# Kernel optimization log

Hardware: AMD Instinct MI355X
Metric: run time of the kernel (lower is better)

Reference implementation:

```python
import jax, jax.numpy as jnp
import numpy as np

DIM_M = 512
NEG_INF = -1e30


def setup_inputs() -> dict:
    key = jax.random.key(0)
    k1, k2, k3, k4, k5, k6, k7 = jax.random.split(key, 7)
    B, Lc, Lq, d = 16, 1024, 512, DIM_M
    C = jax.random.normal(k1, (B, Lc, d), dtype=jnp.float32)
    Q = jax.random.normal(k2, (B, Lq, d), dtype=jnp.float32)
    cmask = jax.random.randint(k3, (B, Lc), 0, 2).astype(jnp.float32)
    qmask = jax.random.randint(k4, (B, Lq), 0, 2).astype(jnp.float32)
    lim = np.sqrt(1.0 / d)
    w = jax.random.uniform(k5, (3 * d,), minval=-lim, maxval=lim, dtype=jnp.float32)
    # out_linear: Linear(4d -> d), torch default init
    bound = np.sqrt(1.0 / (4 * d))
    out_w = jax.random.uniform(k6, (d, 4 * d), minval=-bound, maxval=bound, dtype=jnp.float32)
    out_b = jax.random.uniform(k7, (d,), minval=-bound, maxval=bound, dtype=jnp.float32)
    return {"C": C, "Q": Q, "cmask": cmask, "qmask": qmask, "w": w, "out_w": out_w, "out_b": out_b}


def _mask_logits(t, m):
    return t * m + (1.0 - m) * NEG_INF


def reference(C, Q, cmask, qmask, w, out_w, out_b):
    d = C.shape[-1]
    w1, w2, w3 = w[:d], w[d:2 * d], w[2 * d:]
    # Decomposed trilinear similarity (same math as cat([Ct,Qt,Ct*Qt]) @ w):
    # S[b,i,j] = C[b,i]@w1 + Q[b,j]@w2 + (C[b,i]*w3) @ Q[b,j]
    S = (C @ w1)[:, :, None] + (Q @ w2)[:, None, :] \
        + jnp.einsum('bid,bjd->bij', C * w3, Q)  # [B, Lc, Lq]
    qm = qmask[:, None, :]  # [B, 1, Lq]
    cm = cmask[:, :, None]  # [B, Lc, 1]
    S1 = jax.nn.softmax(_mask_logits(S, qm), axis=2)  # over Lq
    S2 = jax.nn.softmax(_mask_logits(S, cm), axis=1)  # over Lc
    A = jnp.einsum('bij,bjd->bid', S1, Q)  # [B, Lc, d]
    # bmm(bmm(S1, S2^T), C) == S1 @ (S2^T @ C) by associativity (cheaper)
    S2TC = jnp.einsum('bij,bid->bjd', S2, C)  # [B, Lq, d]
    Bm = jnp.einsum('bij,bjd->bid', S1, S2TC)  # [B, Lc, d]
    out = jnp.concatenate([C, A, C * A, C * Bm], axis=2)  # [B, Lc, 4d]
    # dropout inactive (inference); out_linear
    return out @ out_w.T + out_b
```

## Files before the change

### kernel.cpp

```cpp
#include <hip/hip_runtime.h>
#include <hip/hip_bf16.h>


#define NB 16
#define LC 1024
#define LQ 512
#define DM 512
#define D4 2048
#define NEGINF (-1e30f)
#define BK 32
#define LDAp 40

typedef __bf16 v8bf __attribute__((ext_vector_type(8)));
typedef __bf16 v4bf __attribute__((ext_vector_type(4)));
typedef float  v4f  __attribute__((ext_vector_type(4)));

#define MFMA16 __builtin_amdgcn_mfma_f32_16x16x32_bf16

#define TILE_SETUP8 \
  const int t = threadIdx.x, lane = t & 63, wave = t >> 6; \
  const int wm = wave >> 2, wn = wave & 3, quad = lane >> 4, col = lane & 15; \
  const int sr = t >> 2, skc = (t & 3) * 8;

#define ZERO_ACC8 \
  v4f acc[4][2]; \
  _Pragma("unroll") for (int x = 0; x < 4; ++x) \
  _Pragma("unroll") for (int y = 0; y < 2; ++y) \
  _Pragma("unroll") for (int r = 0; r < 4; ++r) acc[x][y][r] = 0.f;

#define FRAG_MMA8(AL, BL) do { \
  v8bf af_[4], bf_[2]; \
  _Pragma("unroll") for (int x = 0; x < 4; ++x) \
    af_[x] = *(const v8bf*)&AL[(wm * 64 + x * 16 + col) * LDAp + quad * 8]; \
  _Pragma("unroll") for (int y = 0; y < 2; ++y) \
    bf_[y] = *(const v8bf*)&BL[(wn * 32 + y * 16 + col) * LDAp + quad * 8]; \
  _Pragma("unroll") for (int x = 0; x < 4; ++x) \
  _Pragma("unroll") for (int y = 0; y < 2; ++y) \
    acc[x][y] = MFMA16(af_[x], bf_[y], acc[x][y], 0, 0, 0); \
} while (0)

__device__ __forceinline__ void xcd_remap(int& bx, int& by, int& bz) {
  const int gx = gridDim.x, gy = gridDim.y, gz = gridDim.z;
  int flat = bx + gx * (by + gy * bz);
  int per = (gx * gy * gz) >> 3;
  int nw = (flat & 7) * per + (flat >> 3);
  bx = nw % gx;
  int r = nw / gx;
  by = r % gy;
  bz = r / gy;
}

__device__ __forceinline__ v8bf cvt8(const float* p) {
  float4 f0 = *(const float4*)p, f1 = *(const float4*)(p + 4);
  v8bf h;
  h[0] = (__bf16)f0.x; h[1] = (__bf16)f0.y; h[2] = (__bf16)f0.z; h[3] = (__bf16)f0.w;
  h[4] = (__bf16)f1.x; h[5] = (__bf16)f1.y; h[6] = (__bf16)f1.z; h[7] = (__bf16)f1.w;
  return h;
}

__global__ void k_rowdots(const float* __restrict__ C, const float* __restrict__ Q,
                          const float* __restrict__ w,
                          float* __restrict__ cw1, float* __restrict__ qw2) {
  const int wid = threadIdx.x >> 6, lane = threadIdx.x & 63;
  const int row = blockIdx.x * 4 + wid;
  const bool isC = row < NB * LC;
  const float* src = isC ? (C + (size_t)row * DM) : (Q + (size_t)(row - NB * LC) * DM);
  const float* wv  = isC ? w : (w + DM);
  float v = 0.f;
#pragma unroll
  for (int tt = 0; tt < 8; ++tt) {
    int k = lane + 64 * tt;
    v += src[k] * wv[k];
  }
#pragma unroll
  for (int off = 32; off; off >>= 1) v += __shfl_down(v, off, 64);
  if (lane == 0) {
    if (isC) cw1[row] = v;
    else     qw2[row - NB * LC] = v;
  }
}

__global__ void k_transpose(const float* __restrict__ in, __bf16* __restrict__ outT,
                            int R, int Cd) {
  __shared__ __bf16 tile[64][66];
  const int b = blockIdx.z;
  const int r0 = blockIdx.y * 64, c0 = blockIdx.x * 64;
  const int tr = threadIdx.x >> 6, tc = threadIdx.x & 63;
  const float* inb = in + (size_t)b * R * Cd;
  __bf16* outb = outT + (size_t)b * Cd * R;
  for (int r = tr; r < 64; r += 4)
    tile[r][tc] = (__bf16)inb[(size_t)(r0 + r) * Cd + c0 + tc];
  __syncthreads();
  for (int c = tr; c < 64; c += 4)
    outb[(size_t)(c0 + c) * R + r0 + tc] = tile[tc][c];
}

__global__ __launch_bounds__(512) void k_mfma_S(
    const float* __restrict__ C, const float* __restrict__ Q, const float* __restrict__ w,
    const float* __restrict__ cw1, const float* __restrict__ qw2, float* __restrict__ S) {
  __shared__ __bf16 Al[128 * LDAp], Bl[128 * LDAp];
  int bx = blockIdx.x, by = blockIdx.y, bz = blockIdx.z;
  xcd_remap(bx, by, bz);
  const int b = bz, i0 = by * 128, j0 = bx * 128;
  TILE_SETUP8
  const float* Cb = C + (size_t)b * LC * DM;
  const float* Qb = Q + (size_t)b * LQ * DM;
  const float* w3 = w + 2 * DM;
  ZERO_ACC8
  for (int k0 = 0; k0 < DM; k0 += BK) {
    const float* ca = Cb + (size_t)(i0 + sr) * DM + k0 + skc;
    const float* qa = Qb + (size_t)(j0 + sr) * DM + k0 + skc;
    const float* wa = w3 + k0 + skc;
    float4 c0 = *(const float4*)ca, c1 = *(const float4*)(ca + 4);
    float4 w0 = *(const float4*)wa, w1 = *(const float4*)(wa + 4);
    v8bf ah;
    ah[0] = (__bf16)(c0.x * w0.x); ah[1] = (__bf16)(c0.y * w0.y);
    ah[2] = (__bf16)(c0.z * w0.z); ah[3] = (__bf16)(c0.w * w0.w);
    ah[4] = (__bf16)(c1.x * w1.x); ah[5] = (__bf16)(c1.y * w1.y);
    ah[6] = (__bf16)(c1.z * w1.z); ah[7] = (__bf16)(c1.w * w1.w);
    *(v8bf*)&Al[sr * LDAp + skc] = ah;
    *(v8bf*)&Bl[sr * LDAp + skc] = cvt8(qa);
    __syncthreads();
    FRAG_MMA8(Al, Bl);
    __syncthreads();
  }
  float* Sb = S + (size_t)b * LC * LQ;
#pragma unroll
  for (int x = 0; x < 4; ++x) {
    const int mB = i0 + wm * 64 + x * 16 + quad * 4;
    float cv[4];
#pragma unroll
    for (int r = 0; r < 4; ++r) cv[r] = cw1[b * LC + mB + r];
#pragma unroll
    for (int y = 0; y < 2; ++y) {
      const int j = j0 + wn * 32 + y * 16 + col;
      const float qv = qw2[b * LQ + j];
#pragma unroll
      for (int r = 0; r < 4; ++r)
        Sb[(size_t)(mB + r) * LQ + j] = acc[x][y][r] + cv[r] + qv;
    }
  }
}

__global__ __launch_bounds__(1024) void k_softstat(
    const float* __restrict__ S, const float* __restrict__ qmask,
    const float* __restrict__ cmask, __bf16* __restrict__ S1,
    float2* __restrict__ pstat) {
  __shared__ float2 cst[16][LQ];
  const int b = blockIdx.y, ic = blockIdx.x;
  const int tid = threadIdx.x, wv = tid >> 6, lane = tid & 63;
  const float* qm  = qmask + b * LQ;
  const float* cm  = cmask + b * LC + ic * 64;
  const float* Sb  = S  + ((size_t)b * LC + ic * 64) * LQ;
  __bf16*      S1b = S1 + ((size_t)b * LC + ic * 64) * LQ;
  float colm[8], cols[8];
#pragma unroll
  for (int tt = 0; tt < 8; ++tt) { colm[tt] = -3e38f; cols[tt] = 0.f; }
  for (int it = 0; it < 4; ++it) {
    const int r = wv * 4 + it;
    const float cmv = cm[r];
    const float* Srow = Sb + (size_t)r * LQ;
    float sv[8], l1[8];
    float m = -3e38f;
#pragma unroll
    for (int tt = 0; tt < 8; ++tt) {
      int j = lane + 64 * tt;
      sv[tt] = Srow[j];
      float qv = qm[j];
      l1[tt] = qv * sv[tt] + (1.f - qv) * NEGINF;
      m = fmaxf(m, l1[tt]);
    }
#pragma unroll
    for (int off = 32; off; off >>= 1) m = fmaxf(m, __shfl_xor(m, off, 64));
    float e[8], s = 0.f;
#pragma unroll
    for (int tt = 0; tt < 8; ++tt) { e[tt] = __expf(l1[tt] - m); s += e[tt]; }
#pragma unroll
    for (int off = 32; off; off >>= 1) s += __shfl_xor(s, off, 64);
    const float inv = 1.f / s;
#pragma unroll
    for (int tt = 0; tt < 8; ++tt)
      S1b[(size_t)r * LQ + lane + 64 * tt] = (__bf16)(e[tt] * inv);
#pragma unroll
    for (int tt = 0; tt < 8; ++tt) {
      float l2 = cmv * sv[tt] + (1.f - cmv) * NEGINF;
      if (l2 > colm[tt]) { cols[tt] *= __expf(colm[tt] - l2); colm[tt] = l2; }
      cols[tt] += __expf(l2 - colm[tt]);
    }
  }
#pragma unroll
  for (int tt = 0; tt < 8; ++tt) cst[wv][lane + 64 * tt] = make_float2(colm[tt], cols[tt]);
  __syncthreads();
  if (tid < LQ) {
    float M = -3e38f, Sd = 0.f;
#pragma unroll
    for (int k = 0; k < 16; ++k) {
      float2 p = cst[k][tid];
      float nM = fmaxf(M, p.x);
      Sd = Sd * __expf(M - nM) + p.y * __expf(p.x - nM);
      M = nM;
    }
    pstat[((size_t)(b * 16 + ic) * LQ) + tid] = make_float2(M, Sd);
  }
}

__global__ void k_colwrite(const float* __restrict__ S, const float* __restrict__ cmask,
                           const float2* __restrict__ pstat, __bf16* __restrict__ S2T) {
  __shared__ float Mf[64], If[64];
  __shared__ __bf16 tile[64][66];
  const int b = blockIdx.z, ic = blockIdx.y, j0 = blockIdx.x * 64;
  const int c = threadIdx.x & 63, ip = threadIdx.x >> 6;
  if (threadIdx.x < 64) {
    float M = -3e38f, Sd = 0.f;
#pragma unroll
    for (int k = 0; k < 16; ++k) {
      float2 p = pstat[((size_t)(b * 16 + k) * LQ) + j0 + threadIdx.x];
      float nM = fmaxf(M, p.x);
      Sd = Sd * __expf(M - nM) + p.y * __expf(p.x - nM);
      M = nM;
    }
    Mf[threadIdx.x] = M; If[threadIdx.x] = 1.f / Sd;
  }
  __syncthreads();
  const float M = Mf[c], inv = If[c];
  const float* Sb = S + ((size_t)b * LC + ic * 64) * LQ;
  const float* cm = cmask + b * LC + ic * 64;
  for (int r = ip; r < 64; r += 4) {
    float mk = cm[r];
    float logit = mk * Sb[(size_t)r * LQ + j0 + c] + (1.f - mk) * NEGINF;
    tile[r][c] = (__bf16)(__expf(logit - M) * inv);
  }
  __syncthreads();
  __bf16* S2Tb = S2T + ((size_t)b * LQ + j0) * LC + ic * 64;
  for (int jr = ip; jr < 64; jr += 4)
    S2Tb[(size_t)jr * LC + c] = tile[c][jr];
}

__global__ __launch_bounds__(512) void k_mfma_A(
    const __bf16* __restrict__ S1, const __bf16* __restrict__ QT, __bf16* __restrict__ Aw) {
  __shared__ __bf16 Al[128 * LDAp], Bl[128 * LDAp];
  int bx = blockIdx.x, by = blockIdx.y, bz = blockIdx.z;
  xcd_remap(bx, by, bz);
  const int b = bz, i0 = by * 128, n0 = bx * 128;
  TILE_SETUP8
  const __bf16* S1b = S1 + (size_t)b * LC * LQ;
  const __bf16* QTb = QT + (size_t)b * DM * LQ;
  ZERO_ACC8
  for (int k0 = 0; k0 < LQ; k0 += BK) {
    *(v8bf*)&Al[sr * LDAp + skc] = *(const v8bf*)(S1b + (size_t)(i0 + sr) * LQ + k0 + skc);
    *(v8bf*)&Bl[sr * LDAp + skc] = *(const v8bf*)(QTb + (size_t)(n0 + sr) * LQ + k0 + skc);
    __syncthreads();
    FRAG_MMA8(Al, Bl);
    __syncthreads();
  }
  __bf16* Ab = Aw + (size_t)b * LC * DM;
#pragma unroll
  for (int x = 0; x < 4; ++x) {
    const int mB = i0 + wm * 64 + x * 16 + quad * 4;
#pragma unroll
    for (int y = 0; y < 2; ++y) {
      const int n = n0 + wn * 32 + y * 16 + col;
#pragma unroll
      for (int r = 0; r < 4; ++r)
        Ab[(size_t)(mB + r) * DM + n] = (__bf16)acc[x][y][r];
    }
  }
}

__global__ __launch_bounds__(512) void k_mfma_T(
    const __bf16* __restrict__ S2T, const __bf16* __restrict__ CT, __bf16* __restrict__ S2TCT) {
  __shared__ __bf16 Al[128 * LDAp], Bl[128 * LDAp];
  int bx = blockIdx.x, by = blockIdx.y, bz = blockIdx.z;
  xcd_remap(bx, by, bz);
  const int b = bz, j0 = by * 128, n0 = bx * 128;
  TILE_SETUP8
  const __bf16* S2Tb = S2T + (size_t)b * LQ * LC;
  const __bf16* CTb  = CT  + (size_t)b * DM * LC;
  ZERO_ACC8
  for (int k0 = 0; k0 < LC; k0 += BK) {
    *(v8bf*)&Al[sr * LDAp + skc] = *(const v8bf*)(S2Tb + (size_t)(j0 + sr) * LC + k0 + skc);
    *(v8bf*)&Bl[sr * LDAp + skc] = *(const v8bf*)(CTb  + (size_t)(n0 + sr) * LC + k0 + skc);
    __syncthreads();
    FRAG_MMA8(Al, Bl);
    __syncthreads();
  }
#pragma unroll
  for (int x = 0; x < 4; ++x) {
    const int jB = j0 + wm * 64 + x * 16 + quad * 4;
#pragma unroll
    for (int y = 0; y < 2; ++y) {
      const int n = n0 + wn * 32 + y * 16 + col;
      v4bf h;
#pragma unroll
      for (int r = 0; r < 4; ++r) h[r] = (__bf16)acc[x][y][r];
      *(v4bf*)&S2TCT[((size_t)b * DM + n) * LQ + jB] = h;
    }
  }
}

__global__ __launch_bounds__(512) void k_mfma_Bm(
    const __bf16* __restrict__ S1, const __bf16* __restrict__ S2TCT, __bf16* __restrict__ Bmw) {
  __shared__ __bf16 Al[128 * LDAp], Bl[128 * LDAp];
  int bx = blockIdx.x, by = blockIdx.y, bz = blockIdx.z;
  xcd_remap(bx, by, bz);
  const int b = bz, i0 = by * 128, n0 = bx * 128;
  TILE_SETUP8
  const __bf16* S1b = S1 + (size_t)b * LC * LQ;
  const __bf16* Tb  = S2TCT + (size_t)b * DM * LQ;
  ZERO_ACC8
  for (int k0 = 0; k0 < LQ; k0 += BK) {
    *(v8bf*)&Al[sr * LDAp + skc] = *(const v8bf*)(S1b + (size_t)(i0 + sr) * LQ + k0 + skc);
    *(v8bf*)&Bl[sr * LDAp + skc] = *(const v8bf*)(Tb  + (size_t)(n0 + sr) * LQ + k0 + skc);
    __syncthreads();
    FRAG_MMA8(Al, Bl);
    __syncthreads();
  }
  __bf16* Bb = Bmw + (size_t)b * LC * DM;
#pragma unroll
  for (int x = 0; x < 4; ++x) {
    const int mB = i0 + wm * 64 + x * 16 + quad * 4;
#pragma unroll
    for (int y = 0; y < 2; ++y) {
      const int n = n0 + wn * 32 + y * 16 + col;
#pragma unroll
      for (int r = 0; r < 4; ++r)
        Bb[(size_t)(mB + r) * DM + n] = (__bf16)acc[x][y][r];
    }
  }
}

__global__ __launch_bounds__(512) void k_mfma_out(
    const float* __restrict__ C, const __bf16* __restrict__ Aw, const __bf16* __restrict__ Bmw,
    const float* __restrict__ OW, const float* __restrict__ ob, float* __restrict__ out) {
  __shared__ __bf16 Asg[2][128 * LDAp], Bsg[2][128 * LDAp];
  int bx = blockIdx.x, by = blockIdx.y, bz = blockIdx.z;
  xcd_remap(bx, by, bz);
  const int b = bz, i0 = by * 128, n0 = bx * 128;
  TILE_SETUP8
  const float*  Cb = C   + (size_t)b * LC * DM;
  const __bf16* Ab = Aw  + (size_t)b * LC * DM;
  const __bf16* Bb = Bmw + (size_t)b * LC * DM;
  ZERO_ACC8
#pragma unroll
  for (int pass = 0; pass < 2; ++pass) {
    for (int kl0 = 0; kl0 < DM; kl0 += BK) {
      const float*  cr = Cb + (size_t)(i0 + sr) * DM + kl0 + skc;
      const __bf16* ap = Ab + (size_t)(i0 + sr) * DM + kl0 + skc;
      const int off = sr * LDAp + skc;
      v8bf av = *(const v8bf*)ap;
      if (pass == 0) {
        *(v8bf*)&Asg[0][off] = cvt8(cr);
        *(v8bf*)&Asg[1][off] = av;
      } else {
        float4 f0 = *(const float4*)cr, f1 = *(const float4*)(cr + 4);
        v8bf bv = *(const v8bf*)(Bb + (size_t)(i0 + sr) * DM + kl0 + skc);
        float cf[8] = {f0.x, f0.y, f0.z, f0.w, f1.x, f1.y, f1.z, f1.w};
        v8bf hCA, hCB;
#pragma unroll
        for (int e = 0; e < 8; ++e) {
          hCA[e] = (__bf16)(cf[e] * (float)av[e]);
          hCB[e] = (__bf16)(cf[e] * (float)bv[e]);
        }
        *(v8bf*)&Asg[0][off] = hCA;
        *(v8bf*)&Asg[1][off] = hCB;
      }
      const float* owr = OW + (size_t)(n0 + sr) * D4 + pass * 2 * DM + kl0 + skc;
      *(v8bf*)&Bsg[0][off] = cvt8(owr);
      *(v8bf*)&Bsg[1][off] = cvt8(owr + DM);
      __syncthreads();
      FRAG_MMA8(Asg[0], Bsg[0]);
      FRAG_MMA8(Asg[1], Bsg[1]);
      __syncthreads();
    }
  }
  float* outb = out + (size_t)b * LC * DM;
#pragma unroll
  for (int x = 0; x < 4; ++x) {
    const int mB = i0 + wm * 64 + x * 16 + quad * 4;
#pragma unroll
    for (int y = 0; y < 2; ++y) {
      const int n = n0 + wn * 32 + y * 16 + col;
      const float bv = ob[n];
#pragma unroll
      for (int r = 0; r < 4; ++r)
        outb[(size_t)(mB + r) * DM + n] = acc[x][y][r] + bv;
    }
  }
}

extern "C" void kernel_launch(void* const* d_in, const int* in_sizes, int n_in,
                              void* d_out, int out_size, void* d_ws, size_t ws_size,
                              hipStream_t stream) {
  const float* C     = (const float*)d_in[0];
  const float* Q     = (const float*)d_in[1];
  const float* cmask = (const float*)d_in[2];
  const float* qmask = (const float*)d_in[3];
  const float* w     = (const float*)d_in[4];
  const float* out_w = (const float*)d_in[5];
  const float* out_b = (const float*)d_in[6];
  float* out = (float*)d_out;

  char* base = (char*)d_ws;
  float*  cw1   = (float*)base;
  float*  qw2   = (float*)(base + 65536);
  char*   R     = base + 131072;
  float*  S     = (float*)R;
  __bf16* Aw    = (__bf16*)R;
  __bf16* CT    = (__bf16*)(R + (16u << 20));
  __bf16* Bmw   = (__bf16*)(R + (16u << 20));
  __bf16* S1    = (__bf16*)(base + 131072 + (32u << 20));
  __bf16* S2T   = (__bf16*)(base + 131072 + (48u << 20));
  char*   Z     = base + 131072 + (64u << 20);
  float2* pstat = (float2*)Z;
  __bf16* QT    = (__bf16*)Z;
  __bf16* S2TCT = (__bf16*)Z;
  (void)in_sizes; (void)n_in; (void)out_size; (void)ws_size;

  k_rowdots<<<(NB * LC + NB * LQ) / 4, 256, 0, stream>>>(C, Q, w, cw1, qw2);
  k_mfma_S<<<dim3(LQ / 128, LC / 128, NB), 512, 0, stream>>>(C, Q, w, cw1, qw2, S);
  k_softstat<<<dim3(LC / 64, NB), 1024, 0, stream>>>(S, qmask, cmask, S1, pstat);
  k_colwrite<<<dim3(LQ / 64, LC / 64, NB), 256, 0, stream>>>(S, cmask, pstat, S2T);
  k_transpose<<<dim3(DM / 64, LQ / 64, NB), 256, 0, stream>>>(Q, QT, LQ, DM);
  k_transpose<<<dim3(DM / 64, LC / 64, NB), 256, 0, stream>>>(C, CT, LC, DM);
  k_mfma_A<<<dim3(DM / 128, LC / 128, NB), 512, 0, stream>>>(S1, QT, Aw);
  k_mfma_T<<<dim3(DM / 128, LQ / 128, NB), 512, 0, stream>>>(S2T, CT, S2TCT);
  k_mfma_Bm<<<dim3(DM / 128, LC / 128, NB), 512, 0, stream>>>(S1, S2TCT, Bmw);
  k_mfma_out<<<dim3(DM / 128, LC / 128, NB), 512, 0, stream>>>(C, Aw, Bmw, out_w, out_b, out);
}
```

Measured before the change: 299.1 us.

## Prefetch next K-tile into registers, widen K-step, pre-convert out_w to bf16

The MFMA GEMM kernels now load the next K-slice from global memory into registers while the current slice is being computed, which overlaps load latency with MFMA work. The S, A, T and Bm kernels move to a 64-wide K step with a larger LDS stride, so they need half as many barriers. The output GEMM is restructured into a single loop over four LDS buffers and reads out_w from a bf16 copy that a new kernel writes into the S2T workspace once S2T is no longer needed. In exchange, the kernels use more registers and more LDS, and each call pays for an extra conversion launch.

```diff
diff --git a/kernel.cpp b/kernel.cpp
--- a/kernel.cpp
+++ b/kernel.cpp
@@ -8,8 +8,8 @@
 #define DM 512
 #define D4 2048
 #define NEGINF (-1e30f)
-#define BK 32
-#define LDAp 40
+#define LDA64 72
+#define LDA32 40
 
 typedef __bf16 v8bf __attribute__((ext_vector_type(8)));
 typedef __bf16 v4bf __attribute__((ext_vector_type(4)));
@@ -20,7 +20,7 @@
 #define TILE_SETUP8 \
   const int t = threadIdx.x, lane = t & 63, wave = t >> 6; \
   const int wm = wave >> 2, wn = wave & 3, quad = lane >> 4, col = lane & 15; \
-  const int sr = t >> 2, skc = (t & 3) * 8;
+  const int sr = t >> 2;
 
 #define ZERO_ACC8 \
   v4f acc[4][2]; \
@@ -28,12 +28,12 @@
   _Pragma("unroll") for (int y = 0; y < 2; ++y) \
   _Pragma("unroll") for (int r = 0; r < 4; ++r) acc[x][y][r] = 0.f;
 
-#define FRAG_MMA8(AL, BL) do { \
+#define FRAG_MMA8S(AL, BL, LDA, KO) do { \
   v8bf af_[4], bf_[2]; \
   _Pragma("unroll") for (int x = 0; x < 4; ++x) \
-    af_[x] = *(const v8bf*)&AL[(wm * 64 + x * 16 + col) * LDAp + quad * 8]; \
+    af_[x] = *(const v8bf*)&AL[(wm * 64 + x * 16 + col) * LDA + KO + quad * 8]; \
   _Pragma("unroll") for (int y = 0; y < 2; ++y) \
-    bf_[y] = *(const v8bf*)&BL[(wn * 32 + y * 16 + col) * LDAp + quad * 8]; \
+    bf_[y] = *(const v8bf*)&BL[(wn * 32 + y * 16 + col) * LDA + KO + quad * 8]; \
   _Pragma("unroll") for (int x = 0; x < 4; ++x) \
   _Pragma("unroll") for (int y = 0; y < 2; ++y) \
     acc[x][y] = MFMA16(af_[x], bf_[y], acc[x][y], 0, 0, 0); \
@@ -50,11 +50,10 @@
   bz = r / gy;
 }
 
-__device__ __forceinline__ v8bf cvt8(const float* p) {
-  float4 f0 = *(const float4*)p, f1 = *(const float4*)(p + 4);
+__device__ __forceinline__ v8bf cvt8f(float4 a, float4 b) {
   v8bf h;
-  h[0] = (__bf16)f0.x; h[1] = (__bf16)f0.y; h[2] = (__bf16)f0.z; h[3] = (__bf16)f0.w;
-  h[4] = (__bf16)f1.x; h[5] = (__bf16)f1.y; h[6] = (__bf16)f1.z; h[7] = (__bf16)f1.w;
+  h[0] = (__bf16)a.x; h[1] = (__bf16)a.y; h[2] = (__bf16)a.z; h[3] = (__bf16)a.w;
+  h[4] = (__bf16)b.x; h[5] = (__bf16)b.y; h[6] = (__bf16)b.z; h[7] = (__bf16)b.w;
   return h;
 }
 
@@ -95,33 +94,56 @@
     outb[(size_t)(c0 + c) * R + r0 + tc] = tile[tc][c];
 }
 
+__global__ void k_owcvt(const float* __restrict__ OW, __bf16* __restrict__ OWb) {
+  size_t i = ((size_t)blockIdx.x * 256 + threadIdx.x) * 4;
+  float4 f = *(const float4*)(OW + i);
+  v4bf h; h[0] = (__bf16)f.x; h[1] = (__bf16)f.y; h[2] = (__bf16)f.z; h[3] = (__bf16)f.w;
+  *(v4bf*)(OWb + i) = h;
+}
+
 __global__ __launch_bounds__(512) void k_mfma_S(
     const float* __restrict__ C, const float* __restrict__ Q, const float* __restrict__ w,
     const float* __restrict__ cw1, const float* __restrict__ qw2, float* __restrict__ S) {
-  __shared__ __bf16 Al[128 * LDAp], Bl[128 * LDAp];
+  __shared__ __bf16 Al[128 * LDA64], Bl[128 * LDA64];
   int bx = blockIdx.x, by = blockIdx.y, bz = blockIdx.z;
   xcd_remap(bx, by, bz);
   const int b = bz, i0 = by * 128, j0 = bx * 128;
   TILE_SETUP8
+  const int skc = (t & 3) * 16;
   const float* Cb = C + (size_t)b * LC * DM;
   const float* Qb = Q + (size_t)b * LQ * DM;
   const float* w3 = w + 2 * DM;
-  ZERO_ACC8
-  for (int k0 = 0; k0 < DM; k0 += BK) {
+  float4 pc[4], pq[4];
+  auto load = [&](int k0) {
     const float* ca = Cb + (size_t)(i0 + sr) * DM + k0 + skc;
     const float* qa = Qb + (size_t)(j0 + sr) * DM + k0 + skc;
+#pragma unroll
+    for (int u = 0; u < 4; ++u) {
+      pc[u] = *(const float4*)(ca + 4 * u);
+      pq[u] = *(const float4*)(qa + 4 * u);
+    }
+  };
+  load(0);
+  ZERO_ACC8
+  for (int k0 = 0; k0 < DM; k0 += 64) {
     const float* wa = w3 + k0 + skc;
-    float4 c0 = *(const float4*)ca, c1 = *(const float4*)(ca + 4);
-    float4 w0 = *(const float4*)wa, w1 = *(const float4*)(wa + 4);
-    v8bf ah;
-    ah[0] = (__bf16)(c0.x * w0.x); ah[1] = (__bf16)(c0.y * w0.y);
-    ah[2] = (__bf16)(c0.z * w0.z); ah[3] = (__bf16)(c0.w * w0.w);
-    ah[4] = (__bf16)(c1.x * w1.x); ah[5] = (__bf16)(c1.y * w1.y);
-    ah[6] = (__bf16)(c1.z * w1.z); ah[7] = (__bf16)(c1.w * w1.w);
-    *(v8bf*)&Al[sr * LDAp + skc] = ah;
-    *(v8bf*)&Bl[sr * LDAp + skc] = cvt8(qa);
-    __syncthreads();
-    FRAG_MMA8(Al, Bl);
+#pragma unroll
+    for (int u = 0; u < 2; ++u) {
+      float4 c0 = pc[2 * u], c1 = pc[2 * u + 1];
+      float4 w0 = *(const float4*)(wa + 8 * u), w1 = *(const float4*)(wa + 8 * u + 4);
+      v8bf ah;
+      ah[0] = (__bf16)(c0.x * w0.x); ah[1] = (__bf16)(c0.y * w0.y);
+      ah[2] = (__bf16)(c0.z * w0.z); ah[3] = (__bf16)(c0.w * w0.w);
+      ah[4] = (__bf16)(c1.x * w1.x); ah[5] = (__bf16)(c1.y * w1.y);
+      ah[6] = (__bf16)(c1.z * w1.z); ah[7] = (__bf16)(c1.w * w1.w);
+      *(v8bf*)&Al[sr * LDA64 + skc + 8 * u] = ah;
+      *(v8bf*)&Bl[sr * LDA64 + skc + 8 * u] = cvt8f(pq[2 * u], pq[2 * u + 1]);
+    }
+    __syncthreads();
+    int kn = k0 + 64; if (kn >= DM) kn = 0;
+    load(kn);
+    FRAG_MMA8S(Al, Bl, LDA64, 0);
+    FRAG_MMA8S(Al, Bl, LDA64, 32);
     __syncthreads();
   }
   float* Sb = S + (size_t)b * LC * LQ;
@@ -238,19 +260,29 @@
 
 __global__ __launch_bounds__(512) void k_mfma_A(
     const __bf16* __restrict__ S1, const __bf16* __restrict__ QT, __bf16* __restrict__ Aw) {
-  __shared__ __bf16 Al[128 * LDAp], Bl[128 * LDAp];
+  __shared__ __bf16 Al[128 * LDA64], Bl[128 * LDA64];
   int bx = blockIdx.x, by = blockIdx.y, bz = blockIdx.z;
   xcd_remap(bx, by, bz);
   const int b = bz, i0 = by * 128, n0 = bx * 128;
   TILE_SETUP8
-  const __bf16* S1b = S1 + (size_t)b * LC * LQ;
-  const __bf16* QTb = QT + (size_t)b * DM * LQ;
+  const int skc = (t & 3) * 16;
+  const __bf16* Ar = S1 + (size_t)b * LC * LQ + (size_t)(i0 + sr) * LQ + skc;
+  const __bf16* Br = QT + (size_t)b * DM * LQ + (size_t)(n0 + sr) * LQ + skc;
+  v8bf pa0, pa1, pb0, pb1;
+  auto load = [&](int k0) {
+    pa0 = *(const v8bf*)(Ar + k0); pa1 = *(const v8bf*)(Ar + k0 + 8);
+    pb0 = *(const v8bf*)(Br + k0); pb1 = *(const v8bf*)(Br + k0 + 8);
+  };
+  load(0);
   ZERO_ACC8
-  for (int k0 = 0; k0 < LQ; k0 += BK) {
-    *(v8bf*)&Al[sr * LDAp + skc] = *(const v8bf*)(S1b + (size_t)(i0 + sr) * LQ + k0 + skc);
-    *(v8bf*)&Bl[sr * LDAp + skc] = *(const v8bf*)(QTb + (size_t)(n0 + sr) * LQ + k0 + skc);
-    __syncthreads();
-    FRAG_MMA8(Al, Bl);
+  for (int k0 = 0; k0 < LQ; k0 += 64) {
+    *(v8bf*)&Al[sr * LDA64 + skc] = pa0; *(v8bf*)&Al[sr * LDA64 + skc + 8] = pa1;
+    *(v8bf*)&Bl[sr * LDA64 + skc] = pb0; *(v8bf*)&Bl[sr * LDA64 + skc + 8] = pb1;
+    __syncthreads();
+    int kn = k0 + 64; if (kn >= LQ) kn = 0;
+    load(kn);
+    FRAG_MMA8S(Al, Bl, LDA64, 0);
+    FRAG_MMA8S(Al, Bl, LDA64, 32);
     __syncthreads();
   }
   __bf16* Ab = Aw + (size_t)b * LC * DM;
@@ -269,19 +301,29 @@
 
 __global__ __launch_bounds__(512) void k_mfma_T(
     const __bf16* __restrict__ S2T, const __bf16* __restrict__ CT, __bf16* __restrict__ S2TCT) {
-  __shared__ __bf16 Al[128 * LDAp], Bl[128 * LDAp];
+  __shared__ __bf16 Al[128 * LDA64], Bl[128 * LDA64];
   int bx = blockIdx.x, by = blockIdx.y, bz = blockIdx.z;
   xcd_remap(bx, by, bz);
   const int b = bz, j0 = by * 128, n0 = bx * 128;
   TILE_SETUP8
-  const __bf16* S2Tb = S2T + (size_t)b * LQ * LC;
-  const __bf16* CTb  = CT  + (size_t)b * DM * LC;
+  const int skc = (t & 3) * 16;
+  const __bf16* Ar = S2T + (size_t)b * LQ * LC + (size_t)(j0 + sr) * LC + skc;
+  const __bf16* Br = CT  + (size_t)b * DM * LC + (size_t)(n0 + sr) * LC + skc;
+  v8bf pa0, pa1, pb0, pb1;
+  auto load = [&](int k0) {
+    pa0 = *(const v8bf*)(Ar + k0); pa1 = *(const v8bf*)(Ar + k0 + 8);
+    pb0 = *(const v8bf*)(Br + k0); pb1 = *(const v8bf*)(Br + k0 + 8);
+  };
+  load(0);
   ZERO_ACC8
-  for (int k0 = 0; k0 < LC; k0 += BK) {
-    *(v8bf*)&Al[sr * LDAp + skc] = *(const v8bf*)(S2Tb + (size_t)(j0 + sr) * LC + k0 + skc);
-    *(v8bf*)&Bl[sr * LDAp + skc] = *(const v8bf*)(CTb  + (size_t)(n0 + sr) * LC + k0 + skc);
-    __syncthreads();
-    FRAG_MMA8(Al, Bl);
+  for (int k0 = 0; k0 < LC; k0 += 64) {
+    *(v8bf*)&Al[sr * LDA64 + skc] = pa0; *(v8bf*)&Al[sr * LDA64 + skc + 8] = pa1;
+    *(v8bf*)&Bl[sr * LDA64 + skc] = pb0; *(v8bf*)&Bl[sr * LDA64 + skc + 8] = pb1;
+    __syncthreads();
+    int kn = k0 + 64; if (kn >= LC) kn = 0;
+    load(kn);
+    FRAG_MMA8S(Al, Bl, LDA64, 0);
+    FRAG_MMA8S(Al, Bl, LDA64, 32);
     __syncthreads();
   }
 #pragma unroll
@@ -300,19 +342,29 @@
 
 __global__ __launch_bounds__(512) void k_mfma_Bm(
     const __bf16* __restrict__ S1, const __bf16* __restrict__ S2TCT, __bf16* __restrict__ Bmw) {
-  __shared__ __bf16 Al[128 * LDAp], Bl[128 * LDAp];
+  __shared__ __bf16 Al[128 * LDA64], Bl[128 * LDA64];
   int bx = blockIdx.x, by = blockIdx.y, bz = blockIdx.z;
   xcd_remap(bx, by, bz);
   const int b = bz, i0 = by * 128, n0 = bx * 128;
   TILE_SETUP8
-  const __bf16* S1b = S1 + (size_t)b * LC * LQ;
-  const __bf16* Tb  = S2TCT + (size_t)b * DM * LQ;
+  const int skc = (t & 3) * 16;
+  const __bf16* Ar = S1    + (size_t)b * LC * LQ + (size_t)(i0 + sr) * LQ + skc;
+  const __bf16* Br = S2TCT + (size_t)b * DM * LQ + (size_t)(n0 + sr) * LQ + skc;
+  v8bf pa0, pa1, pb0, pb1;
+  auto load = [&](int k0) {
+    pa0 = *(const v8bf*)(Ar + k0); pa1 = *(const v8bf*)(Ar + k0 + 8);
+    pb0 = *(const v8bf*)(Br + k0); pb1 = *(const v8bf*)(Br + k0 + 8);
+  };
+  load(0);
   ZERO_ACC8
-  for (int k0 = 0; k0 < LQ; k0 += BK) {
-    *(v8bf*)&Al[sr * LDAp + skc] = *(const v8bf*)(S1b + (size_t)(i0 + sr) * LQ + k0 + skc);
-    *(v8bf*)&Bl[sr * LDAp + skc] = *(const v8bf*)(Tb  + (size_t)(n0 + sr) * LQ + k0 + skc);
-    __syncthreads();
-    FRAG_MMA8(Al, Bl);
+  for (int k0 = 0; k0 < LQ; k0 += 64) {
+    *(v8bf*)&Al[sr * LDA64 + skc] = pa0; *(v8bf*)&Al[sr * LDA64 + skc + 8] = pa1;
+    *(v8bf*)&Bl[sr * LDA64 + skc] = pb0; *(v8bf*)&Bl[sr * LDA64 + skc + 8] = pb1;
+    __syncthreads();
+    int kn = k0 + 64; if (kn >= LQ) kn = 0;
+    load(kn);
+    FRAG_MMA8S(Al, Bl, LDA64, 0);
+    FRAG_MMA8S(Al, Bl, LDA64, 32);
     __syncthreads();
   }
   __bf16* Bb = Bmw + (size_t)b * LC * DM;
@@ -331,47 +383,49 @@
 
 __global__ __launch_bounds__(512) void k_mfma_out(
     const float* __restrict__ C, const __bf16* __restrict__ Aw, const __bf16* __restrict__ Bmw,
-    const float* __restrict__ OW, const float* __restrict__ ob, float* __restrict__ out) {
-  __shared__ __bf16 Asg[2][128 * LDAp], Bsg[2][128 * LDAp];
+    const __bf16* __restrict__ OWb, const float* __restrict__ ob, float* __restrict__ out) {
+  __shared__ __bf16 Asg[4][128 * LDA32], Bsg[4][128 * LDA32];
   int bx = blockIdx.x, by = blockIdx.y, bz = blockIdx.z;
   xcd_remap(bx, by, bz);
   const int b = bz, i0 = by * 128, n0 = bx * 128;
   TILE_SETUP8
-  const float*  Cb = C   + (size_t)b * LC * DM;
-  const __bf16* Ab = Aw  + (size_t)b * LC * DM;
-  const __bf16* Bb = Bmw + (size_t)b * LC * DM;
+  const int skc = (t & 3) * 8;
+  const float*  Cr = C   + (size_t)b * LC * DM + (size_t)(i0 + sr) * DM + skc;
+  const __bf16* Ar = Aw  + (size_t)b * LC * DM + (size_t)(i0 + sr) * DM + skc;
+  const __bf16* Br = Bmw + (size_t)b * LC * DM + (size_t)(i0 + sr) * DM + skc;
+  const __bf16* Wr = OWb + (size_t)(n0 + sr) * D4 + skc;
+  float4 pc0, pc1; v8bf pA, pB, pw[4];
+  auto load = [&](int kl) {
+    pc0 = *(const float4*)(Cr + kl); pc1 = *(const float4*)(Cr + kl + 4);
+    pA = *(const v8bf*)(Ar + kl);
+    pB = *(const v8bf*)(Br + kl);
+#pragma unroll
+    for (int s = 0; s < 4; ++s) pw[s] = *(const v8bf*)(Wr + s * DM + kl);
+  };
+  load(0);
   ZERO_ACC8
-#pragma unroll
-  for (int pass = 0; pass < 2; ++pass) {
-    for (int kl0 = 0; kl0 < DM; kl0 += BK) {
-      const float*  cr = Cb + (size_t)(i0 + sr) * DM + kl0 + skc;
-      const __bf16* ap = Ab + (size_t)(i0 + sr) * DM + kl0 + skc;
-      const int off = sr * LDAp + skc;
-      v8bf av = *(const v8bf*)ap;
-      if (pass == 0) {
-        *(v8bf*)&Asg[0][off] = cvt8(cr);
-        *(v8bf*)&Asg[1][off] = av;
-      } else {
-        float4 f0 = *(const float4*)cr, f1 = *(const float4*)(cr + 4);
-        v8bf bv = *(const v8bf*)(Bb + (size_t)(i0 + sr) * DM + kl0 + skc);
-        float cf[8] = {f0.x, f0.y, f0.z, f0.w, f1.x, f1.y, f1.z, f1.w};
-        v8bf hCA, hCB;
-#pragma unroll
-        for (int e = 0; e < 8; ++e) {
-          hCA[e] = (__bf16)(cf[e] * (float)av[e]);
-          hCB[e] = (__bf16)(cf[e] * (float)bv[e]);
-        }
-        *(v8bf*)&Asg[0][off] = hCA;
-        *(v8bf*)&Asg[1][off] = hCB;
-      }
-      const float* owr = OW + (size_t)(n0 + sr) * D4 + pass * 2 * DM + kl0 + skc;
-      *(v8bf*)&Bsg[0][off] = cvt8(owr);
-      *(v8bf*)&Bsg[1][off] = cvt8(owr + DM);
-      __syncthreads();
-      FRAG_MMA8(Asg[0], Bsg[0]);
-      FRAG_MMA8(Asg[1], Bsg[1]);
-      __syncthreads();
-    }
+  for (int kl = 0; kl < DM; kl += 32) {
+    float cf[8] = {pc0.x, pc0.y, pc0.z, pc0.w, pc1.x, pc1.y, pc1.z, pc1.w};
+    v8bf hC, hCA, hCB;
+#pragma unroll
+    for (int e = 0; e < 8; ++e) {
+      hC[e]  = (__bf16)cf[e];
+      hCA[e] = (__bf16)(cf[e] * (float)pA[e]);
+      hCB[e] = (__bf16)(cf[e] * (float)pB[e]);
+    }
+    const int off = sr * LDA32 + skc;
+    *(v8bf*)&Asg[0][off] = hC;
+    *(v8bf*)&Asg[1][off] = pA;
+    *(v8bf*)&Asg[2][off] = hCA;
+    *(v8bf*)&Asg[3][off] = hCB;
+#pragma unroll
+    for (int s = 0; s < 4; ++s) *(v8bf*)&Bsg[s][off] = pw[s];
+    __syncthreads();
+    int kn = kl + 32; if (kn >= DM) kn = 0;
+    load(kn);
+#pragma unroll
+    for (int s = 0; s < 4; ++s) FRAG_MMA8S(Asg[s], Bsg[s], LDA32, 0);
+    __syncthreads();
   }
   float* outb = out + (size_t)b * LC * DM;
 #pragma unroll
@@ -410,6 +464,7 @@
   __bf16* Bmw   = (__bf16*)(R + (16u << 20));
   __bf16* S1    = (__bf16*)(base + 131072 + (32u << 20));
   __bf16* S2T   = (__bf16*)(base + 131072 + (48u << 20));
+  __bf16* OWbf  = S2T;
   char*   Z     = base + 131072 + (64u << 20);
   float2* pstat = (float2*)Z;
   __bf16* QT    = (__bf16*)Z;
@@ -424,6 +479,7 @@
   k_transpose<<<dim3(DM / 64, LC / 64, NB), 256, 0, stream>>>(C, CT, LC, DM);
   k_mfma_A<<<dim3(DM / 128, LC / 128, NB), 512, 0, stream>>>(S1, QT, Aw);
   k_mfma_T<<<dim3(DM / 128, LQ / 128, NB), 512, 0, stream>>>(S2T, CT, S2TCT);
+  k_owcvt<<<DM * D4 / 1024, 256, 0, stream>>>(out_w, OWbf);
   k_mfma_Bm<<<dim3(DM / 128, LC / 128, NB), 512, 0, stream>>>(S1, S2TCT, Bmw);
-  k_mfma_out<<<dim3(DM / 128, LC / 128, NB), 512, 0, stream>>>(C, Aw, Bmw, out_w, out_b, out);
-}
+  k_mfma_out<<<dim3(DM / 128, LC / 128, NB), 512, 0, stream>>>(C, Aw, Bmw, OWbf, out_b, out);
+}
```

New measurement: 281.1 us. -6.0%, faster.
